# Kernel tuning notes

Hardware: AMD Instinct MI355X
Metric: run time of the kernel (lower is better)

## Reference

```python
import jax, jax.numpy as jnp
import numpy as np

B, T = 1024, 39
NUM_C, NUM_STU, NUM_E, EMB = 123, 100000, 50000, 256
H = 123
IN1 = NUM_C + EMB  # 379


def setup_inputs() -> dict:
    key = jax.random.key(0)
    ks = jax.random.split(key, 32)
    f = lambda k, shp, s: jax.random.normal(k, shp, dtype=jnp.float32) * s
    inp = {}
    inp["q_maritx"] = jax.random.uniform(ks[0], (B, T, NUM_C), dtype=jnp.float32)
    inp["q_maritx_next"] = jax.random.uniform(ks[1], (B, T, NUM_C), dtype=jnp.float32)
    inp["concept"] = jax.random.randint(ks[2], (B, T), 0, NUM_C + 1)
    inp["s_id"] = jax.random.randint(ks[3], (B, 1), 0, NUM_STU + 1)
    inp["e_id"] = jax.random.randint(ks[4], (B, T), 0, NUM_E + 1)
    inp["r"] = jax.random.randint(ks[5], (B, T), 0, 2)
    inp["q_next"] = jax.random.randint(ks[6], (B, T), 0, NUM_E + 1)
    inp["concept_next"] = jax.random.randint(ks[7], (B, T), 0, NUM_C + 1)
    # learned parameters
    inp["emb_problem"] = f(ks[8], (NUM_E + 1, EMB), 1.0)
    inp["student_W"] = f(ks[9], (NUM_STU + 1, NUM_C), 1.0)
    inp["k_diff_W"] = f(ks[10], (NUM_E + 1, NUM_C), 1.0)
    inp["e_disc_W"] = f(ks[11], (NUM_E + 1, 1), 1.0)
    inp["answer_W"] = f(ks[12], (2, EMB), 1.0)
    inp["zz_W"] = f(ks[13], (NUM_C, NUM_C), 0.05)
    inp["zz_b"] = jnp.zeros((NUM_C,), jnp.float32)
    inp["d_t"] = f(ks[14], (1,), 1.0)
    inp["d_e"] = f(ks[15], (1,), 1.0)
    inp["W_ih"] = f(ks[16], (H, IN1), 0.05)
    inp["b_ih"] = jnp.zeros((H,), jnp.float32)
    inp["W_hh"] = f(ks[17], (H, H), 0.05)
    inp["b_hh"] = jnp.zeros((H,), jnp.float32)
    inp["W_tg"] = f(ks[18], (H, 1), 0.05)
    inp["b_tg"] = jnp.zeros((H,), jnp.float32)
    inp["W_z"] = f(ks[19], (H, IN1 + H), 0.05)
    inp["b_z"] = jnp.zeros((H,), jnp.float32)
    inp["W_h"] = f(ks[20], (H, IN1 + H), 0.05)
    inp["b_h"] = jnp.zeros((H,), jnp.float32)
    inp["p1_W"] = f(ks[21], (256, 502), 0.05)
    inp["p1_b"] = jnp.zeros((256,), jnp.float32)
    inp["p2_W"] = f(ks[22], (123, 256), 0.05)
    inp["p2_b"] = jnp.zeros((123,), jnp.float32)
    inp["p3_W"] = f(ks[23], (1, 123), 0.05)
    inp["p3_b"] = jnp.zeros((1,), jnp.float32)
    return inp


def _forward(q_maritx, q_maritx_next, emb_problem, student_W, k_diff_W, e_disc_W,
             answer_W, zz_W, zz_b, d_t, d_e, W_ih, b_ih, W_hh, b_hh, W_tg, b_tg,
             W_z, b_z, W_h, b_h, p1_W, p1_b, p2_W, p2_b, p3_W, p3_b,
             s_id, e_id, r, q_next):
    Bc, Tc = e_id.shape
    e_next_emb = emb_problem[q_next]                       # [B,T,256]
    s_prof = jax.nn.sigmoid(student_W[s_id])               # [B,1,123] (broadcasts vs repeat(1,39,1))
    k_diff = jax.nn.sigmoid(k_diff_W[e_id])                # [B,T,123]
    e_disc = jax.nn.sigmoid(e_disc_W[e_id]) * d_e          # [B,T,1]
    r_emb = answer_W[r]                                    # [B,T,256]
    concept_ab = jnp.einsum('btk,hk->bth', q_maritx, zz_W) + zz_b  # [B,T,123]
    x1 = jnp.concatenate([concept_ab * s_prof, r_emb], axis=-1)    # [B,T,379]
    # --- time-gated RNN: h_t = tanh(W_ih x_t + W_hh h + b) * sigmoid(tg(t)) ---
    Xp = jnp.einsum('bti,hi->bth', x1, W_ih) + b_ih
    tvec = jnp.arange(Tc, dtype=Xp.dtype)[:, None]
    gates = jax.nn.sigmoid(tvec * W_tg[:, 0][None, :] + b_tg)      # [T,123]
    h0 = jnp.zeros((Bc, W_hh.shape[0]), Xp.dtype)

    def step1(h, xs):
        xp, g = xs
        h = jnp.tanh(xp + h @ W_hh.T + b_hh) * g
        return h, h

    _, ys1 = jax.lax.scan(step1, h0, (Xp.transpose(1, 0, 2), gates))
    out_zz = ys1.transpose(1, 0, 2)                        # [B,T,123]
    # --- GRU-like cell (W_r unused in original forward) ---
    input_x1 = e_disc * (d_t * s_prof + (1.0 - d_t) * out_zz - k_diff) * q_maritx
    x2 = jnp.concatenate([input_x1, r_emb], axis=-1)       # [B,T,379]
    nin = x2.shape[-1]
    Wz_x, Wz_h = W_z[:, :nin], W_z[:, nin:]
    Wh_x, Wh_h = W_h[:, :nin], W_h[:, nin:]
    Zx = jnp.einsum('bti,hi->bth', x2, Wz_x) + b_z
    Hx = jnp.einsum('bti,hi->bth', x2, Wh_x) + b_h

    def step2(h, xs):
        zx, hx = xs
        z = jax.nn.sigmoid(zx + h @ Wz_h.T)
        ht = jnp.tanh(hx + h @ Wh_h.T)
        h = (1.0 - z) * h + z * ht
        return h, h

    _, ys2 = jax.lax.scan(step2, h0, (Zx.transpose(1, 0, 2), Hx.transpose(1, 0, 2)))
    outputs = ys2.transpose(1, 0, 2)                       # [B,T,123]
    hcat = jnp.concatenate([outputs, e_next_emb, q_maritx_next], axis=-1)  # [B,T,502]
    o1 = jax.nn.sigmoid(hcat @ p1_W.T + p1_b)  # dropout as identity (deterministic reference)
    o2 = jax.nn.sigmoid(o1 @ p2_W.T + p2_b)
    return jax.nn.sigmoid(o2 @ p3_W.T + p3_b)              # [B,T,1]


def reference(q_maritx, q_maritx_next, emb_problem, student_W, k_diff_W, e_disc_W,
              answer_W, zz_W, zz_b, d_t, d_e, W_ih, b_ih, W_hh, b_hh, W_tg, b_tg,
              W_z, b_z, W_h, b_h, p1_W, p1_b, p2_W, p2_b, p3_W, p3_b,
              concept, s_id, e_id, r, q_next, concept_next):
    # concept / concept_next embeddings are computed but unused in the original output
    return _forward(q_maritx, q_maritx_next, emb_problem, student_W, k_diff_W,
                    e_disc_W, answer_W, zz_W, zz_b, d_t, d_e, W_ih, b_ih, W_hh,
                    b_hh, W_tg, b_tg, W_z, b_z, W_h, b_h, p1_W, p1_b, p2_W,
                    p2_b, p3_W, p3_b, s_id, e_id, r, q_next)
```

## Files before the change

kernel.cpp:

```cpp
#include <hip/hip_runtime.h>
#include <hip/hip_bf16.h>

#define NRB 39936
#define BB 1024
#define TT 39
#define CC 123
#define EMBD 256
#define PCH 136

typedef __attribute__((ext_vector_type(8))) short short8;
typedef __attribute__((ext_vector_type(4))) short shortv4;
typedef __attribute__((ext_vector_type(4))) float floatx4;
typedef unsigned short us;

__device__ __forceinline__ float rcp_(float x){ return __builtin_amdgcn_rcpf(x); }
__device__ __forceinline__ float fsig(float x){ return rcp_(1.f + __expf(-x)); }
__device__ __forceinline__ float ftanh(float x){
  float ax = __builtin_fabsf(x);
  float e = __expf(-2.f*ax);
  float r = (1.f - e) * rcp_(1.f + e);
  return __builtin_copysignf(r, x);
}
__device__ __forceinline__ us f2bf(float x){
  union { float f; unsigned u; } v; v.f = x;
  unsigned r = v.u + 0x7FFFu + ((v.u >> 16) & 1u);
  return (us)(r >> 16);
}
__device__ __forceinline__ us f2bfh(float x){
  __bf16 h = (__bf16)x;
  return __builtin_bit_cast(us, h);
}
__device__ __forceinline__ float bf2f(us u){
  union { unsigned u; float f; } v; v.u = ((unsigned)u) << 16; return v.f;
}

__device__ __forceinline__ void gl_lds16(void* lds, const void* g){
  __builtin_amdgcn_global_load_lds(
      (const __attribute__((address_space(1))) unsigned int*)g,
      (__attribute__((address_space(3))) unsigned int*)lds, 16, 0, 0);
}

#define G_RC 6
#define G_CW 1088
#define G_CAST 2496
#define G_HCAT 1872
#define G_PRE (G_RC + G_CW + G_CAST + G_HCAT)

__global__ __launch_bounds__(256) void k_pre(
    const float* __restrict__ W_ih, const float* __restrict__ W_z,
    const float* __restrict__ W_h, const float* __restrict__ answer_W,
    const float* __restrict__ zz_W, const float* __restrict__ W_hh,
    const float* __restrict__ p1_W, const float* __restrict__ p2_W,
    const float* __restrict__ emb, const int* __restrict__ q_next,
    const float* __restrict__ qmn, const float* __restrict__ q_m,
    float* __restrict__ rtab, us* __restrict__ wts,
    us* __restrict__ p1bf, us* __restrict__ p2bf,
    us* __restrict__ qbf, us* __restrict__ Abf)
{
  const int blk = blockIdx.x, tid = threadIdx.x;
  if (blk < G_RC){
    int which = blk >> 1, j = blk & 1, h = tid;
    if (h >= CC) return;
    const float* W; int stride;
    if (which==0){ W=W_ih; stride=379; } else if (which==1){ W=W_z; stride=502; } else { W=W_h; stride=502; }
    const float* a = answer_W + j*EMBD;
    const float* w = W + (size_t)h*stride + CC;
    float acc = 0.f;
    #pragma unroll 8
    for (int i=0;i<EMBD;i++) acc += w[i]*a[i];
    rtab[(which*2+j)*128 + h] = acc;
    return;
  }
  if (blk < G_RC + G_CW){
    int i = (blk - G_RC)*256 + tid;
    if (i < 7*16384){
      int w = i >> 14, idx = i & 16383, n = idx >> 7, k = idx & 127;
      float v = 0.f;
      if (n < CC && k < CC){
        if      (w==0) v = zz_W[n*CC + k];
        else if (w==1) v = W_ih[n*379 + k];
        else if (w==2) v = W_z [n*502 + k];
        else if (w==3) v = W_h [n*502 + k];
        else if (w==4) v = W_hh[n*CC + k];
        else if (w==5) v = W_z [n*502 + 379 + k];
        else           v = W_h [n*502 + 379 + k];
      }
      wts[i] = f2bf(v);
      return;
    }
    int j = i - 7*16384;
    if (j < 256*512){
      int n = j >> 9, k = j & 511;
      float v;
      if      (k < 379) v = p1_W[n*502 + k + 123];
      else if (k < 384) v = 0.f;
      else if (k < 507) v = p1_W[n*502 + (k - 384)];
      else              v = 0.f;
      p1bf[j] = f2bf(v);
      return;
    }
    j -= 256*512;
    if (j < 128*256){
      int n = j >> 8, k = j & 255;
      p2bf[j] = f2bf(n < CC ? p2_W[n*256 + k] : 0.f);
    }
    return;
  }
  if (blk < G_RC + G_CW + G_CAST){
    const size_t total = (size_t)NRB*128;
    for (size_t i = (size_t)(blk - G_RC - G_CW)*256 + tid; i < total; i += (size_t)G_CAST*256){
      int col = (int)(i & 127); size_t rp = i >> 7;
      int t = (int)(rp >> 10), b = (int)(rp & 1023);
      float v = (col < CC) ? q_m[((size_t)b*TT + t)*CC + col] : 0.f;
      qbf[i] = f2bf(v);
    }
    return;
  }
  {
    const size_t nchunk = (size_t)NRB*48;
    for (size_t c = (size_t)(blk - G_RC - G_CW - G_CAST)*256 + tid; c < nchunk; c += (size_t)G_HCAT*256){
      size_t row = c / 48;
      int c0 = (int)(c - row*48) * 8;
      short8 o;
      if (c0 < 256){
        int qn = q_next[row];
        float4 v0 = *(const float4*)(emb + (size_t)qn*EMBD + c0);
        float4 v1 = *(const float4*)(emb + (size_t)qn*EMBD + c0 + 4);
        o[0]=f2bf(v0.x); o[1]=f2bf(v0.y); o[2]=f2bf(v0.z); o[3]=f2bf(v0.w);
        o[4]=f2bf(v1.x); o[5]=f2bf(v1.y); o[6]=f2bf(v1.z); o[7]=f2bf(v1.w);
      } else {
        int j0 = c0 - 256;
        #pragma unroll
        for (int jj=0;jj<8;jj++){
          int j = j0 + jj;
          o[jj] = (j < CC) ? f2bf(qmn[row*CC + j]) : (short)0;
        }
      }
      *(short8*)(Abf + row*512 + c0) = o;
    }
  }
}

__global__ __launch_bounds__(256) void k_zz_elem(
    const us* __restrict__ X, const us* __restrict__ W,
    const us* __restrict__ Wih,
    const float* __restrict__ zz_b,
    const float* __restrict__ q_m, const int* __restrict__ s_id,
    const int* __restrict__ e_id, const float* __restrict__ student_W,
    const float* __restrict__ k_diff_W, const float* __restrict__ e_disc_W,
    const float* __restrict__ d_t_p, const float* __restrict__ d_e_p,
    us* __restrict__ xpa, us* __restrict__ xpb,
    us* __restrict__ pre2, us* __restrict__ cqb)
{
  __shared__ __align__(16) us Asl[16][64][8];
  us* x1l = &Asl[0][0][0];
  const int tid = threadIdx.x, w = tid >> 6, l = tid & 63, q = l >> 4, r16 = l & 15;
  const int rTile = blockIdx.x*64;
  const int tbase = rTile >> 4;
  short8 bfr[2][4], bfr2[2][4];
  #pragma unroll
  for (int nt=0;nt<2;nt++){
    int n = w*32 + nt*16 + r16;
    #pragma unroll
    for (int kt=0;kt<4;kt++){
      bfr[nt][kt]  = *(const short8*)(W   + (size_t)n*128 + kt*32 + q*8);
      bfr2[nt][kt] = *(const short8*)(Wih + (size_t)n*128 + kt*32 + q*8);
    }
  }
  #pragma unroll
  for (int i=0;i<4;i++){
    int seg = i*4 + w;
    gl_lds16(&Asl[seg][l][0], X + (size_t)(rTile+l)*128 + seg*8);
  }
  floatx4 acc[4][2];
  #pragma unroll
  for (int mt=0;mt<4;mt++){
    #pragma unroll
    for (int nt=0;nt<2;nt++){ acc[mt][nt][0]=0.f; acc[mt][nt][1]=0.f; acc[mt][nt][2]=0.f; acc[mt][nt][3]=0.f; }
  }
  __syncthreads();
  #pragma unroll
  for (int kt=0;kt<4;kt++){
    short8 af[4];
    #pragma unroll
    for (int mt=0;mt<4;mt++) af[mt] = *(const short8*)&Asl[kt*4+q][mt*16+r16][0];
    #pragma unroll
    for (int mt=0;mt<4;mt++){
      #pragma unroll
      for (int nt=0;nt<2;nt++)
        acc[mt][nt] = __builtin_amdgcn_mfma_f32_16x16x32_bf16(af[mt], bfr[nt][kt], acc[mt][nt], 0,0,0);
    }
  }
  __syncthreads();
  const float dt = d_t_p[0], de = d_e_p[0];
  float zzb[2]; int colv[2];
  #pragma unroll
  for (int nt=0;nt<2;nt++){
    int col = w*32 + nt*16 + r16; colv[nt] = col;
    zzb[nt] = (col < CC) ? zz_b[col] : 0.f;
  }
  const int t = rTile >> 10;
  #pragma unroll
  for (int mt=0;mt<4;mt++){
    #pragma unroll
    for (int i=0;i<4;i++){
      int row = rTile + mt*16 + q*4 + i;
      int b = row & 1023;
      int g = b*TT + t;
      int btile = b >> 4, r = b & 15;
      int sid = s_id[b];
      int e   = e_id[g];
      float ed = fsig(e_disc_W[e]) * de;
      size_t base = ((size_t)t*64 + btile)*2048;
      #pragma unroll
      for (int nt=0;nt<2;nt++){
        int col = colv[nt];
        float x1v = 0.f, p2v = 0.f, cqv = 0.f;
        if (col < CC){
          float ab = acc[mt][nt][i] + zzb[nt];
          float sp = fsig(student_W[(size_t)sid*CC + col]);
          float kd = fsig(k_diff_W[(size_t)e*CC + col]);
          float qv = q_m[(size_t)g*CC + col];
          x1v = ab*sp;
          p2v = ed*(dt*sp - kd)*qv;
          cqv = ed*(1.f - dt)*qv;
        }
        x1l[mt*2048 + (w*64 + (nt*2 + (r16>>3))*16 + (q*4+i))*8 + (r16&7)] = f2bf(x1v);
        size_t off = base + (size_t)(((col>>5)*64 + ((r>>2))*16 + (col&15))*8) + ((col>>4)&1)*4 + (r&3);
        pre2[off] = f2bf(p2v);
        cqb[off]  = f2bf(cqv);
      }
    }
  }
  __syncthreads();
  floatx4 ac2[4][2];
  #pragma unroll
  for (int mt=0;mt<4;mt++){
    #pragma unroll
    for (int nt=0;nt<2;nt++){ ac2[mt][nt][0]=0.f; ac2[mt][nt][1]=0.f; ac2[mt][nt][2]=0.f; ac2[mt][nt][3]=0.f; }
  }
  #pragma unroll
  for (int kt=0;kt<4;kt++){
    short8 af[4];
    #pragma unroll
    for (int mt=0;mt<4;mt++)
      af[mt] = *(const short8*)&x1l[mt*2048 + (size_t)(kt*64 + q*16 + r16)*8];
    #pragma unroll
    for (int mt=0;mt<4;mt++){
      #pragma unroll
      for (int nt=0;nt<2;nt++)
        ac2[mt][nt] = __builtin_amdgcn_mfma_f32_16x16x32_bf16(af[mt], bfr2[nt][kt], ac2[mt][nt], 0,0,0);
    }
  }
  #pragma unroll
  for (int mt=0;mt<4;mt++){
    #pragma unroll
    for (int nt=0;nt<2;nt++){
      int col = w*32 + nt*16 + r16;
      float* fb = (col < 64) ? (float*)(xpa + (size_t)(tbase+mt)*2048)
                             : (float*)(xpb + (size_t)(tbase+mt)*2048);
      *(floatx4*)(fb + (size_t)(col & 63)*16 + q*4) = ac2[mt][nt];
    }
  }
}

__global__ __launch_bounds__(512,1) void k_mid(
    const us* __restrict__ xpa, const us* __restrict__ xpb,
    const us* __restrict__ pre2, const us* __restrict__ cqb,
    const us* __restrict__ Whh,
    const us* __restrict__ Wzx, const us* __restrict__ Whx,
    const us* __restrict__ Wzh, const us* __restrict__ Whh2,
    const float* __restrict__ b_ih, const float* __restrict__ b_z, const float* __restrict__ b_h,
    const float* __restrict__ W_tg, const float* __restrict__ b_tg,
    const float* __restrict__ rtab, const int* __restrict__ r_idx,
    us* __restrict__ Abf)
{
  __shared__ __align__(16) us h1s[2][16*PCH];
  __shared__ __align__(16) us x2s[2][16*PCH];
  __shared__ __align__(16) us h2s[2][16*PCH];
  __shared__ int rint[TT*16];

  const int tid = threadIdx.x, wid = tid >> 6, l = tid & 63, q = l >> 4, r16 = l & 15;
  const bool isA = wid < 4;
  const int gw = wid & 3;
  const int bbase = blockIdx.x*16;
  const int n0 = gw*32 + r16, n1 = n0 + 16;

  short8 w[4][2][4];
  if (isA){
    #pragma unroll
    for (int tt=0;tt<2;tt++){
      const int nn = n0 + tt*16;
      #pragma unroll
      for (int kt=0;kt<4;kt++)
        w[0][tt][kt] = *(const short8*)(Whh + (size_t)nn*128 + kt*32 + q*8);
    }
  } else {
    #pragma unroll
    for (int tt=0;tt<2;tt++){
      const int nn = n0 + tt*16;
      #pragma unroll
      for (int kt=0;kt<4;kt++){
        size_t wofs = (size_t)nn*128 + kt*32 + q*8;
        w[0][tt][kt] = *(const short8*)(Wzx + wofs);
        w[1][tt][kt] = *(const short8*)(Wzh + wofs);
        w[2][tt][kt] = *(const short8*)(Whx + wofs);
        w[3][tt][kt] = *(const short8*)(Whh2 + wofs);
      }
    }
  }

  const bool v0 = n0 < CC, v1 = n1 < CC;
  float ia0[2], ia1[2], ib0[2], ib1[2];
  float wg0=0.f, bg0=0.f, wg1=0.f, bg1=0.f;
  if (isA){
    ia0[0] = v0 ? b_ih[n0] + rtab[n0]     : 0.f;
    ia1[0] = v0 ? b_ih[n0] + rtab[128+n0] : 0.f;
    ia0[1] = v1 ? b_ih[n1] + rtab[n1]     : 0.f;
    ia1[1] = v1 ? b_ih[n1] + rtab[128+n1] : 0.f;
    ib0[0]=0.f; ib1[0]=0.f; ib0[1]=0.f; ib1[1]=0.f;
    wg0 = v0 ? W_tg[n0]:0.f; bg0 = v0 ? b_tg[n0]:0.f;
    wg1 = v1 ? W_tg[n1]:0.f; bg1 = v1 ? b_tg[n1]:0.f;
  } else {
    ia0[0] = v0 ? b_z[n0] + rtab[256+n0] : 0.f;
    ia1[0] = v0 ? b_z[n0] + rtab[384+n0] : 0.f;
    ia0[1] = v1 ? b_z[n1] + rtab[256+n1] : 0.f;
    ia1[1] = v1 ? b_z[n1] + rtab[384+n1] : 0.f;
    ib0[0] = v0 ? b_h[n0] + rtab[512+n0] : 0.f;
    ib1[0] = v0 ? b_h[n0] + rtab[640+n0] : 0.f;
    ib0[1] = v1 ? b_h[n1] + rtab[512+n1] : 0.f;
    ib1[1] = v1 ? b_h[n1] + rtab[640+n1] : 0.f;
  }

  for (int i = tid; i < TT*16; i += 512)
    rint[i] = r_idx[(size_t)(bbase + (i & 15))*TT + (i >> 4)];
  for (int i = tid; i < 16*PCH; i += 512){ h1s[1][i] = 0; h2s[1][i] = 0; }

  const float* xpbase = (gw < 2) ? (const float*)xpa : (const float*)xpb;
  const int xoff = (((gw&1)*32 + r16)*16 + q*4);

  float4 xc0, xc1; short8 pc8, cc8;
  if (isA){
    const float* fb = xpbase + (size_t)blockIdx.x*1024 + xoff;
    xc0 = *(const float4*)fb;
    xc1 = *(const float4*)(fb + 256);
    size_t cofs = (size_t)blockIdx.x*2048 + (size_t)(gw*64 + q*16 + r16)*8;
    pc8 = *(const short8*)(pre2 + cofs);
    cc8 = *(const short8*)(cqb + cofs);
  }
  __syncthreads();

  floatx4 hold0, hold1;
  hold0[0]=0.f; hold0[1]=0.f; hold0[2]=0.f; hold0[3]=0.f;
  hold1[0]=0.f; hold1[1]=0.f; hold1[2]=0.f; hold1[3]=0.f;

  for (int k=0; k<=TT; ++k){
    const int pA = k & 1;
    if (isA){
      float4 xn0, xn1; short8 pcn, ccn;
      if (k+1 < TT){
        size_t tnext = (size_t)(k+1)*64 + blockIdx.x;
        const float* fb = xpbase + tnext*1024 + xoff;
        xn0 = *(const float4*)fb;
        xn1 = *(const float4*)(fb + 256);
        size_t cofs = tnext*2048 + (size_t)(gw*64 + q*16 + r16)*8;
        pcn = *(const short8*)(pre2 + cofs);
        ccn = *(const short8*)(cqb + cofs);
      }
      if (k < TT){
        short8 fr1[4];
        #pragma unroll
        for (int kt=0;kt<4;kt++)
          fr1[kt] = *(const short8*)&h1s[pA^1][r16*PCH + kt*32 + q*8];
        int4 rs = *(const int4*)&rint[k*16 + q*4];
        floatx4 a0, a1;
        a0[0] = (rs.x ? ia1[0] : ia0[0]) + xc0.x;  a1[0] = (rs.x ? ia1[1] : ia0[1]) + xc1.x;
        a0[1] = (rs.y ? ia1[0] : ia0[0]) + xc0.y;  a1[1] = (rs.y ? ia1[1] : ia0[1]) + xc1.y;
        a0[2] = (rs.z ? ia1[0] : ia0[0]) + xc0.z;  a1[2] = (rs.z ? ia1[1] : ia0[1]) + xc1.z;
        a0[3] = (rs.w ? ia1[0] : ia0[0]) + xc0.w;  a1[3] = (rs.w ? ia1[1] : ia0[1]) + xc1.w;
        #pragma unroll
        for (int kt=0;kt<4;kt++){
          a0 = __builtin_amdgcn_mfma_f32_16x16x32_bf16(fr1[kt], w[0][0][kt], a0, 0,0,0);
          a1 = __builtin_amdgcn_mfma_f32_16x16x32_bf16(fr1[kt], w[0][1][kt], a1, 0,0,0);
        }
        float g0 = fsig((float)k*wg0 + bg0);
        float g1 = fsig((float)k*wg1 + bg1);
        #pragma unroll
        for (int i=0;i<4;i++){
          float h1v0 = ftanh(a0[i]) * g0;
          h1s[pA][(q*4+i)*PCH + n0] = f2bfh(h1v0);
          x2s[pA][(q*4+i)*PCH + n0] = f2bfh(bf2f((us)pc8[i]) + bf2f((us)cc8[i])*h1v0);
          float h1v1 = ftanh(a1[i]) * g1;
          h1s[pA][(q*4+i)*PCH + n1] = f2bfh(h1v1);
          x2s[pA][(q*4+i)*PCH + n1] = f2bfh(bf2f((us)pc8[4+i]) + bf2f((us)cc8[4+i])*h1v1);
        }
      }
      if (k >= 2){
        int row = tid >> 4, cs = tid & 15;
        short8 hv8 = *(const short8*)&h2s[pA][row*PCH + cs*8];
        *(short8*)(Abf + ((size_t)(bbase + row)*TT + (k-2))*512 + 384 + cs*8) = hv8;
      }
      if (k+1 < TT){ xc0 = xn0; xc1 = xn1; pc8 = pcn; cc8 = ccn; }
    } else if (k >= 1){
      const int t = k-1, pB = t & 1;
      short8 fx[4], fh[4];
      #pragma unroll
      for (int kt=0;kt<4;kt++){
        int sidx = r16*PCH + kt*32 + q*8;
        fx[kt] = *(const short8*)&x2s[pB][sidx];
        fh[kt] = *(const short8*)&h2s[pB^1][sidx];
      }
      int4 rs = *(const int4*)&rint[t*16 + q*4];
      floatx4 az0, az1, ah0, ah1;
      az0[0] = rs.x ? ia1[0] : ia0[0];  ah0[0] = rs.x ? ib1[0] : ib0[0];
      az0[1] = rs.y ? ia1[0] : ia0[0];  ah0[1] = rs.y ? ib1[0] : ib0[0];
      az0[2] = rs.z ? ia1[0] : ia0[0];  ah0[2] = rs.z ? ib1[0] : ib0[0];
      az0[3] = rs.w ? ia1[0] : ia0[0];  ah0[3] = rs.w ? ib1[0] : ib0[0];
      az1[0] = rs.x ? ia1[1] : ia0[1];  ah1[0] = rs.x ? ib1[1] : ib0[1];
      az1[1] = rs.y ? ia1[1] : ia0[1];  ah1[1] = rs.y ? ib1[1] : ib0[1];
      az1[2] = rs.z ? ia1[1] : ia0[1];  ah1[2] = rs.z ? ib1[1] : ib0[1];
      az1[3] = rs.w ? ia1[1] : ia0[1];  ah1[3] = rs.w ? ib1[1] : ib0[1];
      #pragma unroll
      for (int kt=0;kt<4;kt++){
        az0 = __builtin_amdgcn_mfma_f32_16x16x32_bf16(fx[kt], w[0][0][kt], az0, 0,0,0);
        az0 = __builtin_amdgcn_mfma_f32_16x16x32_bf16(fh[kt], w[1][0][kt], az0, 0,0,0);
        ah0 = __builtin_amdgcn_mfma_f32_16x16x32_bf16(fx[kt], w[2][0][kt], ah0, 0,0,0);
        ah0 = __builtin_amdgcn_mfma_f32_16x16x32_bf16(fh[kt], w[3][0][kt], ah0, 0,0,0);
        az1 = __builtin_amdgcn_mfma_f32_16x16x32_bf16(fx[kt], w[0][1][kt], az1, 0,0,0);
        az1 = __builtin_amdgcn_mfma_f32_16x16x32_bf16(fh[kt], w[1][1][kt], az1, 0,0,0);
        ah1 = __builtin_amdgcn_mfma_f32_16x16x32_bf16(fx[kt], w[2][1][kt], ah1, 0,0,0);
        ah1 = __builtin_amdgcn_mfma_f32_16x16x32_bf16(fh[kt], w[3][1][kt], ah1, 0,0,0);
      }
      #pragma unroll
      for (int i=0;i<4;i++){
        float z0  = fsig(az0[i]);
        float th0 = ftanh(ah0[i]);
        hold0[i] += z0*(th0 - hold0[i]);
        h2s[pB][(q*4+i)*PCH + n0] = f2bfh(hold0[i]);
        float z1  = fsig(az1[i]);
        float th1 = ftanh(ah1[i]);
        hold1[i] += z1*(th1 - hold1[i]);
        h2s[pB][(q*4+i)*PCH + n1] = f2bfh(hold1[i]);
      }
    }
    __syncthreads();
  }
  if (tid < 256){
    int row = tid >> 4, cs = tid & 15;
    short8 hv8 = *(const short8*)&h2s[(TT-1)&1][row*PCH + cs*8];
    *(short8*)(Abf + ((size_t)(bbase + row)*TT + (TT-1))*512 + 384 + cs*8) = hv8;
  }
}

__global__ __launch_bounds__(256) void k_out(
    const us* __restrict__ Abf, const us* __restrict__ p1bf,
    const float* __restrict__ p1_b, const us* __restrict__ p2bf,
    const float* __restrict__ p2_b, const float* __restrict__ p3_W,
    const float* __restrict__ p3_b, float* __restrict__ out)
{
  __shared__ __align__(16) us smem[20480];
  __shared__ float red[64][4];
  us* Asl = smem;
  us* Bsl = smem + 4096;
  us* o1s = smem;
  const int tid = threadIdx.x;
  const int w = tid >> 6, l = tid & 63;
  const int q = l >> 4, r16 = l & 15;
  const int rTile = blockIdx.x * 64;
  floatx4 acc[4][4];
  #pragma unroll
  for (int a=0;a<4;a++){
    #pragma unroll
    for (int b=0;b<4;b++){ acc[a][b][0]=0.f; acc[a][b][1]=0.f; acc[a][b][2]=0.f; acc[a][b][3]=0.f; }
  }
  for (int c = 0; c < 8; c++){
    const int k0 = c*64;
    #pragma unroll
    for (int i=0;i<2;i++){
      int u = i*256 + tid; int seg = u>>6, m = u&63;
      gl_lds16(&Asl[(seg*64 + m)*8], Abf + (size_t)(rTile+m)*512 + k0 + seg*8);
    }
    #pragma unroll
    for (int i=0;i<8;i++){
      int u = i*256 + tid; int seg = u>>8, nn = u&255;
      gl_lds16(&Bsl[(seg*256 + nn)*8], p1bf + (size_t)nn*512 + k0 + seg*8);
    }
    __syncthreads();
    #pragma unroll
    for (int ks=0; ks<2; ks++){
      int seg = ks*4 + q;
      short8 af[4], bfr[4];
      #pragma unroll
      for (int mt=0;mt<4;mt++) af[mt] = *(const short8*)&Asl[(seg*64 + mt*16 + r16)*8];
      #pragma unroll
      for (int nt=0;nt<4;nt++) bfr[nt] = *(const short8*)&Bsl[(seg*256 + w*64 + nt*16 + r16)*8];
      #pragma unroll
      for (int mt=0;mt<4;mt++){
        #pragma unroll
        for (int nt=0;nt<4;nt++)
          acc[mt][nt] = __builtin_amdgcn_mfma_f32_16x16x32_bf16(af[mt], bfr[nt], acc[mt][nt], 0,0,0);
      }
    }
    __syncthreads();
  }
  #pragma unroll
  for (int nt=0;nt<4;nt++){
    int col = w*64 + nt*16 + r16;
    float bb = p1_b[col];
    #pragma unroll
    for (int mt=0;mt<4;mt++){
      #pragma unroll
      for (int i=0;i<4;i++)
        o1s[(mt*16 + q*4 + i)*264 + col] = f2bf(fsig(acc[mt][nt][i] + bb));
    }
  }
  __syncthreads();
  short8 bf2[2][8];
  #pragma unroll
  for (int nt=0;nt<2;nt++){
    int n2 = w*32 + nt*16 + r16;
    #pragma unroll
    for (int kt=0;kt<8;kt++)
      bf2[nt][kt] = *(const short8*)(p2bf + (size_t)n2*256 + kt*32 + q*8);
  }
  floatx4 ac2[4][2];
  #pragma unroll
  for (int mt=0;mt<4;mt++){
    #pragma unroll
    for (int nt=0;nt<2;nt++){ ac2[mt][nt][0]=0.f; ac2[mt][nt][1]=0.f; ac2[mt][nt][2]=0.f; ac2[mt][nt][3]=0.f; }
  }
  #pragma unroll
  for (int kt=0;kt<8;kt++){
    short8 af[4];
    #pragma unroll
    for (int mt=0;mt<4;mt++) af[mt] = *(const short8*)&o1s[(mt*16 + r16)*264 + kt*32 + q*8];
    #pragma unroll
    for (int mt=0;mt<4;mt++){
      #pragma unroll
      for (int nt=0;nt<2;nt++)
        ac2[mt][nt] = __builtin_amdgcn_mfma_f32_16x16x32_bf16(af[mt], bf2[nt][kt], ac2[mt][nt], 0,0,0);
    }
  }
  const int n0 = w*32 + r16, n1 = n0 + 16;
  const float pb0 = (n0<CC)? p2_b[n0]:0.f, pb1 = (n1<CC)? p2_b[n1]:0.f;
  const float p30 = (n0<CC)? p3_W[n0]:0.f, p31 = (n1<CC)? p3_W[n1]:0.f;
  #pragma unroll
  for (int mt=0;mt<4;mt++){
    #pragma unroll
    for (int i=0;i<4;i++){
      float s = fsig(ac2[mt][0][i]+pb0)*p30 + fsig(ac2[mt][1][i]+pb1)*p31;
      s += __shfl_xor(s,1,16); s += __shfl_xor(s,2,16);
      s += __shfl_xor(s,4,16); s += __shfl_xor(s,8,16);
      if (r16==0) red[mt*16 + q*4 + i][w] = s;
    }
  }
  __syncthreads();
  if (tid < 64){
    float o = red[tid][0]+red[tid][1]+red[tid][2]+red[tid][3] + p3_b[0];
    out[rTile + tid] = fsig(o);
  }
}

extern "C" void kernel_launch(void* const* d_in, const int* in_sizes, int n_in,
                              void* d_out, int out_size, void* d_ws, size_t ws_size,
                              hipStream_t stream) {
  const float* q_m       = (const float*)d_in[0];
  const float* q_m_next  = (const float*)d_in[1];
  const int*   s_id      = (const int*)d_in[3];
  const int*   e_id      = (const int*)d_in[4];
  const int*   r_idx     = (const int*)d_in[5];
  const int*   q_next    = (const int*)d_in[6];
  const float* emb_problem = (const float*)d_in[8];
  const float* student_W = (const float*)d_in[9];
  const float* k_diff_W  = (const float*)d_in[10];
  const float* e_disc_W  = (const float*)d_in[11];
  const float* answer_W  = (const float*)d_in[12];
  const float* zz_W      = (const float*)d_in[13];
  const float* zz_b      = (const float*)d_in[14];
  const float* d_t       = (const float*)d_in[15];
  const float* d_e       = (const float*)d_in[16];
  const float* W_ih      = (const float*)d_in[17];
  const float* b_ih      = (const float*)d_in[18];
  const float* W_hh      = (const float*)d_in[19];
  const float* W_tg      = (const float*)d_in[21];
  const float* b_tg      = (const float*)d_in[22];
  const float* W_z       = (const float*)d_in[23];
  const float* b_z       = (const float*)d_in[24];
  const float* W_h       = (const float*)d_in[25];
  const float* b_h       = (const float*)d_in[26];
  const float* p1_W      = (const float*)d_in[27];
  const float* p1_b      = (const float*)d_in[28];
  const float* p2_W      = (const float*)d_in[29];
  const float* p2_b      = (const float*)d_in[30];
  const float* p3_W      = (const float*)d_in[31];
  const float* p3_b      = (const float*)d_in[32];

  float* ws   = (float*)d_ws;
  float* rtab = ws;
  us* qbf  = (us*)(ws + 1024);
  us* x1a  = qbf  + (size_t)NRB*128;
  us* pre2 = x1a  + (size_t)NRB*128;
  us* cqb  = pre2 + (size_t)NRB*128;
  us* Abf  = cqb  + (size_t)NRB*128;
  us* wts  = Abf  + (size_t)NRB*512;
  us* p1bf = wts  + 7*16384;
  us* p2bf = p1bf + 256*512;

  const us* zzWbf  = wts + 0*16384;
  const us* Wih123 = wts + 1*16384;
  const us* Wz123  = wts + 2*16384;
  const us* Wh123  = wts + 3*16384;
  const us* Whhbf  = wts + 4*16384;
  const us* Wzhbf  = wts + 5*16384;
  const us* Whh2bf = wts + 6*16384;

  hipLaunchKernelGGL(k_pre, dim3(G_PRE), dim3(256), 0, stream,
                     W_ih, W_z, W_h, answer_W, zz_W, W_hh, p1_W, p2_W,
                     emb_problem, q_next, q_m_next, q_m,
                     rtab, wts, p1bf, p2bf, qbf, Abf);
  hipLaunchKernelGGL(k_zz_elem, dim3(NRB/64), dim3(256), 0, stream,
                     qbf, zzWbf, Wih123, zz_b, q_m, s_id, e_id, student_W, k_diff_W,
                     e_disc_W, d_t, d_e, x1a, qbf, pre2, cqb);
  hipLaunchKernelGGL(k_mid, dim3(BB/16), dim3(512), 0, stream,
                     x1a, qbf, pre2, cqb, Whhbf, Wz123, Wh123, Wzhbf, Whh2bf,
                     b_ih, b_z, b_h, W_tg, b_tg, rtab, r_idx, Abf);
  hipLaunchKernelGGL(k_out, dim3(NRB/64), dim3(256), 0, stream,
                     Abf, p1bf, p1_b, p2bf, p2_b, p3_W, p3_b, (float*)d_out);
}
```

Baseline: 374.1 us.

## Fuse q_m bf16 cast into zz kernel and overlap hcat gather with recurrence

The separate pre-pass that cast q_m to a bf16 staging buffer is removed. The zz/elementwise kernel now reads q_m in fp32 and converts it directly into shared memory, which saves one full write and re-read of a large intermediate. The embedding/q_next gather that builds the output-MLP input moves from k_pre into extra blocks of k_mid, so it can run alongside the 64 latency-bound recurrence blocks. The risk is that those extra 512-thread blocks compete with the recurrence blocks for bandwidth and compute units, and the bf16 buffer now holds a different tensor.

```diff
diff --git a/kernel.cpp b/kernel.cpp
--- a/kernel.cpp
+++ b/kernel.cpp
@@ -42,20 +42,16 @@
 
 #define G_RC 6
 #define G_CW 1088
-#define G_CAST 2496
-#define G_HCAT 1872
-#define G_PRE (G_RC + G_CW + G_CAST + G_HCAT)
+#define G_PRE (G_RC + G_CW)
+#define G_HC2 936
 
 __global__ __launch_bounds__(256) void k_pre(
     const float* __restrict__ W_ih, const float* __restrict__ W_z,
     const float* __restrict__ W_h, const float* __restrict__ answer_W,
     const float* __restrict__ zz_W, const float* __restrict__ W_hh,
     const float* __restrict__ p1_W, const float* __restrict__ p2_W,
-    const float* __restrict__ emb, const int* __restrict__ q_next,
-    const float* __restrict__ qmn, const float* __restrict__ q_m,
     float* __restrict__ rtab, us* __restrict__ wts,
-    us* __restrict__ p1bf, us* __restrict__ p2bf,
-    us* __restrict__ qbf, us* __restrict__ Abf)
+    us* __restrict__ p1bf, us* __restrict__ p2bf)
 {
   const int blk = blockIdx.x, tid = threadIdx.x;
   if (blk < G_RC){
@@ -71,7 +67,7 @@
     rtab[(which*2+j)*128 + h] = acc;
     return;
   }
-  if (blk < G_RC + G_CW){
+  {
     int i = (blk - G_RC)*256 + tid;
     if (i < 7*16384){
       int w = i >> 14, idx = i & 16383, n = idx >> 7, k = idx & 127;
@@ -104,21 +100,164 @@
       int n = j >> 8, k = j & 255;
       p2bf[j] = f2bf(n < CC ? p2_W[n*256 + k] : 0.f);
     }
-    return;
-  }
-  if (blk < G_RC + G_CW + G_CAST){
-    const size_t total = (size_t)NRB*128;
-    for (size_t i = (size_t)(blk - G_RC - G_CW)*256 + tid; i < total; i += (size_t)G_CAST*256){
-      int col = (int)(i & 127); size_t rp = i >> 7;
-      int t = (int)(rp >> 10), b = (int)(rp & 1023);
-      float v = (col < CC) ? q_m[((size_t)b*TT + t)*CC + col] : 0.f;
-      qbf[i] = f2bf(v);
-    }
-    return;
+  }
+}
+
+__global__ __launch_bounds__(256) void k_zz_elem(
+    const us* __restrict__ W, const us* __restrict__ Wih,
+    const float* __restrict__ zz_b,
+    const float* __restrict__ q_m, const int* __restrict__ s_id,
+    const int* __restrict__ e_id, const float* __restrict__ student_W,
+    const float* __restrict__ k_diff_W, const float* __restrict__ e_disc_W,
+    const float* __restrict__ d_t_p, const float* __restrict__ d_e_p,
+    us* __restrict__ xpa, us* __restrict__ xpb,
+    us* __restrict__ pre2, us* __restrict__ cqb)
+{
+  __shared__ __align__(16) us Asl[16][64][8];
+  us* x1l = &Asl[0][0][0];
+  const int tid = threadIdx.x, w = tid >> 6, l = tid & 63, q = l >> 4, r16 = l & 15;
+  const int rTile = blockIdx.x*64;
+  const int tbase = rTile >> 4;
+  const int t = rTile >> 10;
+  short8 bfr[2][4], bfr2[2][4];
+  #pragma unroll
+  for (int nt=0;nt<2;nt++){
+    int n = w*32 + nt*16 + r16;
+    #pragma unroll
+    for (int kt=0;kt<4;kt++){
+      bfr[nt][kt]  = *(const short8*)(W   + (size_t)n*128 + kt*32 + q*8);
+      bfr2[nt][kt] = *(const short8*)(Wih + (size_t)n*128 + kt*32 + q*8);
+    }
   }
   {
+    int b = (rTile + l) & 1023;
+    const float* qrow = q_m + (size_t)(b*TT + t)*CC;
+    #pragma unroll
+    for (int it=0; it<4; ++it){
+      int ch = w*4 + it;
+      int c0 = ch*8;
+      short8 o;
+      #pragma unroll
+      for (int j=0;j<8;j++){
+        int col = c0 + j;
+        o[j] = (col < CC) ? f2bf(qrow[col]) : (short)0;
+      }
+      *(short8*)&Asl[ch][l][0] = o;
+    }
+  }
+  floatx4 acc[4][2];
+  #pragma unroll
+  for (int mt=0;mt<4;mt++){
+    #pragma unroll
+    for (int nt=0;nt<2;nt++){ acc[mt][nt][0]=0.f; acc[mt][nt][1]=0.f; acc[mt][nt][2]=0.f; acc[mt][nt][3]=0.f; }
+  }
+  __syncthreads();
+  #pragma unroll
+  for (int kt=0;kt<4;kt++){
+    short8 af[4];
+    #pragma unroll
+    for (int mt=0;mt<4;mt++) af[mt] = *(const short8*)&Asl[kt*4+q][mt*16+r16][0];
+    #pragma unroll
+    for (int mt=0;mt<4;mt++){
+      #pragma unroll
+      for (int nt=0;nt<2;nt++)
+        acc[mt][nt] = __builtin_amdgcn_mfma_f32_16x16x32_bf16(af[mt], bfr[nt][kt], acc[mt][nt], 0,0,0);
+    }
+  }
+  __syncthreads();
+  const float dt = d_t_p[0], de = d_e_p[0];
+  float zzb[2]; int colv[2];
+  #pragma unroll
+  for (int nt=0;nt<2;nt++){
+    int col = w*32 + nt*16 + r16; colv[nt] = col;
+    zzb[nt] = (col < CC) ? zz_b[col] : 0.f;
+  }
+  #pragma unroll
+  for (int mt=0;mt<4;mt++){
+    #pragma unroll
+    for (int i=0;i<4;i++){
+      int row = rTile + mt*16 + q*4 + i;
+      int b = row & 1023;
+      int g = b*TT + t;
+      int btile = b >> 4, r = b & 15;
+      int sid = s_id[b];
+      int e   = e_id[g];
+      float ed = fsig(e_disc_W[e]) * de;
+      size_t base = ((size_t)t*64 + btile)*2048;
+      #pragma unroll
+      for (int nt=0;nt<2;nt++){
+        int col = colv[nt];
+        float x1v = 0.f, p2v = 0.f, cqv = 0.f;
+        if (col < CC){
+          float ab = acc[mt][nt][i] + zzb[nt];
+          float sp = fsig(student_W[(size_t)sid*CC + col]);
+          float kd = fsig(k_diff_W[(size_t)e*CC + col]);
+          float qv = q_m[(size_t)g*CC + col];
+          x1v = ab*sp;
+          p2v = ed*(dt*sp - kd)*qv;
+          cqv = ed*(1.f - dt)*qv;
+        }
+        x1l[mt*2048 + (w*64 + (nt*2 + (r16>>3))*16 + (q*4+i))*8 + (r16&7)] = f2bf(x1v);
+        size_t off = base + (size_t)(((col>>5)*64 + ((r>>2))*16 + (col&15))*8) + ((col>>4)&1)*4 + (r&3);
+        pre2[off] = f2bf(p2v);
+        cqb[off]  = f2bf(cqv);
+      }
+    }
+  }
+  __syncthreads();
+  floatx4 ac2[4][2];
+  #pragma unroll
+  for (int mt=0;mt<4;mt++){
+    #pragma unroll
+    for (int nt=0;nt<2;nt++){ ac2[mt][nt][0]=0.f; ac2[mt][nt][1]=0.f; ac2[mt][nt][2]=0.f; ac2[mt][nt][3]=0.f; }
+  }
+  #pragma unroll
+  for (int kt=0;kt<4;kt++){
+    short8 af[4];
+    #pragma unroll
+    for (int mt=0;mt<4;mt++)
+      af[mt] = *(const short8*)&x1l[mt*2048 + (size_t)(kt*64 + q*16 + r16)*8];
+    #pragma unroll
+    for (int mt=0;mt<4;mt++){
+      #pragma unroll
+      for (int nt=0;nt<2;nt++)
+        ac2[mt][nt] = __builtin_amdgcn_mfma_f32_16x16x32_bf16(af[mt], bfr2[nt][kt], ac2[mt][nt], 0,0,0);
+    }
+  }
+  #pragma unroll
+  for (int mt=0;mt<4;mt++){
+    #pragma unroll
+    for (int nt=0;nt<2;nt++){
+      int col = w*32 + nt*16 + r16;
+      float* fb = (col < 64) ? (float*)(xpa + (size_t)(tbase+mt)*2048)
+                             : (float*)(xpb + (size_t)(tbase+mt)*2048);
+      *(floatx4*)(fb + (size_t)(col & 63)*16 + q*4) = ac2[mt][nt];
+    }
+  }
+}
+
+__global__ __launch_bounds__(512,1) void k_mid(
+    const us* __restrict__ xpa, const us* __restrict__ xpb,
+    const us* __restrict__ pre2, const us* __restrict__ cqb,
+    const us* __restrict__ Whh,
+    const us* __restrict__ Wzx, const us* __restrict__ Whx,
+    const us* __restrict__ Wzh, const us* __restrict__ Whh2,
+    const float* __restrict__ b_ih, const float* __restrict__ b_z, const float* __restrict__ b_h,
+    const float* __restrict__ W_tg, const float* __restrict__ b_tg,
+    const float* __restrict__ rtab, const int* __restrict__ r_idx,
+    const float* __restrict__ emb, const int* __restrict__ q_next,
+    const float* __restrict__ qmn,
+    us* __restrict__ Abf)
+{
+  __shared__ __align__(16) us h1s[2][16*PCH];
+  __shared__ __align__(16) us x2s[2][16*PCH];
+  __shared__ __align__(16) us h2s[2][16*PCH];
+  __shared__ int rint[TT*16];
+
+  if (blockIdx.x >= 64){
+    const int tid = threadIdx.x;
     const size_t nchunk = (size_t)NRB*48;
-    for (size_t c = (size_t)(blk - G_RC - G_CW - G_CAST)*256 + tid; c < nchunk; c += (size_t)G_HCAT*256){
+    for (size_t c = (size_t)(blockIdx.x-64)*512 + tid; c < nchunk; c += (size_t)G_HC2*512){
       size_t row = c / 48;
       int c0 = (int)(c - row*48) * 8;
       short8 o;
@@ -138,147 +277,8 @@
       }
       *(short8*)(Abf + row*512 + c0) = o;
     }
-  }
-}
-
-__global__ __launch_bounds__(256) void k_zz_elem(
-    const us* __restrict__ X, const us* __restrict__ W,
-    const us* __restrict__ Wih,
-    const float* __restrict__ zz_b,
-    const float* __restrict__ q_m, const int* __restrict__ s_id,
-    const int* __restrict__ e_id, const float* __restrict__ student_W,
-    const float* __restrict__ k_diff_W, const float* __restrict__ e_disc_W,
-    const float* __restrict__ d_t_p, const float* __restrict__ d_e_p,
-    us* __restrict__ xpa, us* __restrict__ xpb,
-    us* __restrict__ pre2, us* __restrict__ cqb)
-{
-  __shared__ __align__(16) us Asl[16][64][8];
-  us* x1l = &Asl[0][0][0];
-  const int tid = threadIdx.x, w = tid >> 6, l = tid & 63, q = l >> 4, r16 = l & 15;
-  const int rTile = blockIdx.x*64;
-  const int tbase = rTile >> 4;
-  short8 bfr[2][4], bfr2[2][4];
-  #pragma unroll
-  for (int nt=0;nt<2;nt++){
-    int n = w*32 + nt*16 + r16;
-    #pragma unroll
-    for (int kt=0;kt<4;kt++){
-      bfr[nt][kt]  = *(const short8*)(W   + (size_t)n*128 + kt*32 + q*8);
-      bfr2[nt][kt] = *(const short8*)(Wih + (size_t)n*128 + kt*32 + q*8);
-    }
-  }
-  #pragma unroll
-  for (int i=0;i<4;i++){
-    int seg = i*4 + w;
-    gl_lds16(&Asl[seg][l][0], X + (size_t)(rTile+l)*128 + seg*8);
-  }
-  floatx4 acc[4][2];
-  #pragma unroll
-  for (int mt=0;mt<4;mt++){
-    #pragma unroll
-    for (int nt=0;nt<2;nt++){ acc[mt][nt][0]=0.f; acc[mt][nt][1]=0.f; acc[mt][nt][2]=0.f; acc[mt][nt][3]=0.f; }
-  }
-  __syncthreads();
-  #pragma unroll
-  for (int kt=0;kt<4;kt++){
-    short8 af[4];
-    #pragma unroll
-    for (int mt=0;mt<4;mt++) af[mt] = *(const short8*)&Asl[kt*4+q][mt*16+r16][0];
-    #pragma unroll
-    for (int mt=0;mt<4;mt++){
-      #pragma unroll
-      for (int nt=0;nt<2;nt++)
-        acc[mt][nt] = __builtin_amdgcn_mfma_f32_16x16x32_bf16(af[mt], bfr[nt][kt], acc[mt][nt], 0,0,0);
-    }
-  }
-  __syncthreads();
-  const float dt = d_t_p[0], de = d_e_p[0];
-  float zzb[2]; int colv[2];
-  #pragma unroll
-  for (int nt=0;nt<2;nt++){
-    int col = w*32 + nt*16 + r16; colv[nt] = col;
-    zzb[nt] = (col < CC) ? zz_b[col] : 0.f;
-  }
-  const int t = rTile >> 10;
-  #pragma unroll
-  for (int mt=0;mt<4;mt++){
-    #pragma unroll
-    for (int i=0;i<4;i++){
-      int row = rTile + mt*16 + q*4 + i;
-      int b = row & 1023;
-      int g = b*TT + t;
-      int btile = b >> 4, r = b & 15;
-      int sid = s_id[b];
-      int e   = e_id[g];
-      float ed = fsig(e_disc_W[e]) * de;
-      size_t base = ((size_t)t*64 + btile)*2048;
-      #pragma unroll
-      for (int nt=0;nt<2;nt++){
-        int col = colv[nt];
-        float x1v = 0.f, p2v = 0.f, cqv = 0.f;
-        if (col < CC){
-          float ab = acc[mt][nt][i] + zzb[nt];
-          float sp = fsig(student_W[(size_t)sid*CC + col]);
-          float kd = fsig(k_diff_W[(size_t)e*CC + col]);
-          float qv = q_m[(size_t)g*CC + col];
-          x1v = ab*sp;
-          p2v = ed*(dt*sp - kd)*qv;
-          cqv = ed*(1.f - dt)*qv;
-        }
-        x1l[mt*2048 + (w*64 + (nt*2 + (r16>>3))*16 + (q*4+i))*8 + (r16&7)] = f2bf(x1v);
-        size_t off = base + (size_t)(((col>>5)*64 + ((r>>2))*16 + (col&15))*8) + ((col>>4)&1)*4 + (r&3);
-        pre2[off] = f2bf(p2v);
-        cqb[off]  = f2bf(cqv);
-      }
-    }
-  }
-  __syncthreads();
-  floatx4 ac2[4][2];
-  #pragma unroll
-  for (int mt=0;mt<4;mt++){
-    #pragma unroll
-    for (int nt=0;nt<2;nt++){ ac2[mt][nt][0]=0.f; ac2[mt][nt][1]=0.f; ac2[mt][nt][2]=0.f; ac2[mt][nt][3]=0.f; }
-  }
-  #pragma unroll
-  for (int kt=0;kt<4;kt++){
-    short8 af[4];
-    #pragma unroll
-    for (int mt=0;mt<4;mt++)
-      af[mt] = *(const short8*)&x1l[mt*2048 + (size_t)(kt*64 + q*16 + r16)*8];
-    #pragma unroll
-    for (int mt=0;mt<4;mt++){
-      #pragma unroll
-      for (int nt=0;nt<2;nt++)
-        ac2[mt][nt] = __builtin_amdgcn_mfma_f32_16x16x32_bf16(af[mt], bfr2[nt][kt], ac2[mt][nt], 0,0,0);
-    }
-  }
-  #pragma unroll
-  for (int mt=0;mt<4;mt++){
-    #pragma unroll
-    for (int nt=0;nt<2;nt++){
-      int col = w*32 + nt*16 + r16;
-      float* fb = (col < 64) ? (float*)(xpa + (size_t)(tbase+mt)*2048)
-                             : (float*)(xpb + (size_t)(tbase+mt)*2048);
-      *(floatx4*)(fb + (size_t)(col & 63)*16 + q*4) = ac2[mt][nt];
-    }
-  }
-}
-
-__global__ __launch_bounds__(512,1) void k_mid(
-    const us* __restrict__ xpa, const us* __restrict__ xpb,
-    const us* __restrict__ pre2, const us* __restrict__ cqb,
-    const us* __restrict__ Whh,
-    const us* __restrict__ Wzx, const us* __restrict__ Whx,
-    const us* __restrict__ Wzh, const us* __restrict__ Whh2,
-    const float* __restrict__ b_ih, const float* __restrict__ b_z, const float* __restrict__ b_h,
-    const float* __restrict__ W_tg, const float* __restrict__ b_tg,
-    const float* __restrict__ rtab, const int* __restrict__ r_idx,
-    us* __restrict__ Abf)
-{
-  __shared__ __align__(16) us h1s[2][16*PCH];
-  __shared__ __align__(16) us x2s[2][16*PCH];
-  __shared__ __align__(16) us h2s[2][16*PCH];
-  __shared__ int rint[TT*16];
+    return;
+  }
 
   const int tid = threadIdx.x, wid = tid >> 6, l = tid & 63, q = l >> 4, r16 = l & 15;
   const bool isA = wid < 4;
@@ -616,14 +616,14 @@
 
   hipLaunchKernelGGL(k_pre, dim3(G_PRE), dim3(256), 0, stream,
                      W_ih, W_z, W_h, answer_W, zz_W, W_hh, p1_W, p2_W,
-                     emb_problem, q_next, q_m_next, q_m,
-                     rtab, wts, p1bf, p2bf, qbf, Abf);
+                     rtab, wts, p1bf, p2bf);
   hipLaunchKernelGGL(k_zz_elem, dim3(NRB/64), dim3(256), 0, stream,
-                     qbf, zzWbf, Wih123, zz_b, q_m, s_id, e_id, student_W, k_diff_W,
+                     zzWbf, Wih123, zz_b, q_m, s_id, e_id, student_W, k_diff_W,
                      e_disc_W, d_t, d_e, x1a, qbf, pre2, cqb);
-  hipLaunchKernelGGL(k_mid, dim3(BB/16), dim3(512), 0, stream,
+  hipLaunchKernelGGL(k_mid, dim3(64 + G_HC2), dim3(512), 0, stream,
                      x1a, qbf, pre2, cqb, Whhbf, Wz123, Wh123, Wzhbf, Whh2bf,
-                     b_ih, b_z, b_h, W_tg, b_tg, rtab, r_idx, Abf);
+                     b_ih, b_z, b_h, W_tg, b_tg, rtab, r_idx,
+                     emb_problem, q_next, q_m_next, Abf);
   hipLaunchKernelGGL(k_out, dim3(NRB/64), dim3(256), 0, stream,
                      Abf, p1bf, p1_b, p2bf, p2_b, p3_W, p3_b, (float*)d_out);
 }
```

New measurement: 390.8 us. 1.04x slower.
